# Optimization experiments

Measured on AMD Instinct MI355X. Metric: run time of the kernel, lower is better.

## Reference

```python
import jax, jax.numpy as jnp
import numpy as np
from jax import lax

D = 30   # embedding_dim (hardcoded in repo)
Q = 30   # question length
N = 4000 # number of sentences in doc
S = 100  # tokens per sentence
K = 5    # k_for_maxpool
SLOPE = 0.1  # LeakyReLU negative slope


def setup_inputs() -> dict:
    key = jax.random.key(0)
    ks = jax.random.split(key, 20)
    rn = lambda k, sh: jax.random.normal(k, sh, dtype=jnp.float32)
    ru = lambda k, sh: jax.random.uniform(k, sh, dtype=jnp.float32)
    return {
        "doc_sents_embeds": rn(ks[0], (N, S, D)),
        "sents_gaf": ru(ks[1], (N, 3)),
        "question_embeds": rn(ks[2], (Q, D)),
        "q_idfs": ru(ks[3], (Q, 1)),
        "doc_gaf": ru(ks[4], (4,)),
        "conv1_w": rn(ks[5], (D, D, 3)) * 0.1,
        "conv1_b": rn(ks[6], (D,)) * 0.1,
        "conv2_w": rn(ks[7], (D, D, 3)) * 0.1,
        "conv2_b": rn(ks[8], (D,)) * 0.1,
        "qw_W": rn(ks[9], (1, D + 1)) * 0.1,
        "qw_b": rn(ks[10], (1,)) * 0.1,
        "lq1_W": rn(ks[11], (8, 6)) * 0.1,
        "lq1_b": rn(ks[12], (8,)) * 0.1,
        "lq2_W": rn(ks[13], (1, 8)) * 0.1,
        "lq2_b": rn(ks[14], (1,)) * 0.1,
        "so_W": rn(ks[15], (1, 4)) * 0.1,
        "so_b": rn(ks[16], (1,)) * 0.1,
        "fl_W": rn(ks[17], (1, 5)) * 0.1,
        "fl_b": rn(ks[18], (1,)) * 0.1,
    }


def _leaky(x):
    return jnp.where(x >= 0, x, SLOPE * x)


def _conv_block(x, w, b):
    # x: [B, L, D]. torch Conv1d(D, D, 3, padding=2) then slice [1:L+1]
    # is exactly a 'same' conv with padding 1 on each side; then residual add.
    y = lax.conv_general_dilated(x.transpose(0, 2, 1), w, (1,), [(1, 1)],
                                 dimension_numbers=("NCH", "OIH", "NCH"))
    y = _leaky(y + b[None, :, None])
    return y.transpose(0, 2, 1) + x


def _cos_sim(A, B):
    # A: [Q, D], B: [N, S, D] -> [N, Q, S] (num/den as in torch my_cosine_sim)
    num = jnp.einsum("qd,nsd->nqs", A, B)
    den = jnp.linalg.norm(A, axis=-1)[None, :, None] * jnp.linalg.norm(B, axis=-1)[:, None, :]
    return num / den


def _pool(sim):
    # sort-based k-max pooling -> [max, avg_of_top_k]; sim: [N, Q, S] -> [N, Q, 2]
    vals = lax.top_k(sim, K)[0]  # descending
    return jnp.stack([vals[..., 0], vals.mean(-1)], axis=-1)


def reference(doc_sents_embeds, sents_gaf, question_embeds, q_idfs, doc_gaf,
              conv1_w, conv1_b, conv2_w, conv2_b, qw_W, qw_b,
              lq1_W, lq1_b, lq2_W, lq2_b, so_W, so_b, fl_W, fl_b):
    # question context (two residual trigram convs)
    q_conv = _conv_block(question_embeds[None], conv1_w, conv1_b)
    q_conv = _conv_block(q_conv, conv2_w, conv2_b)[0]          # [Q, D]
    # question term weights
    qw_in = jnp.concatenate([q_conv, q_idfs], axis=-1)          # [Q, D+1]
    q_weights = jax.nn.softmax((qw_in @ qw_W.T + qw_b)[:, 0])   # [Q]
    # sentence context convs (batched over all sentences)
    conv_res = _conv_block(doc_sents_embeds, conv1_w, conv1_b)
    conv_res = _conv_block(conv_res, conv2_w, conv2_b)          # [N, S, D]
    # similarity matrices
    sim_insens = _cos_sim(question_embeds, doc_sents_embeds)    # [N, Q, S]
    sim_oh = (sim_insens > 1.0 - 1e-3).astype(sim_insens.dtype)
    sim_sens = _cos_sim(q_conv, conv_res)
    # k-max pooling and per-q tiny MLP attention
    feats = jnp.concatenate([_pool(sim_oh), _pool(sim_insens), _pool(sim_sens)], axis=-1)  # [N, Q, 6]
    lo = _leaky(feats @ lq1_W.T + lq1_b) @ lq2_W.T + lq2_b      # [N, Q, 1]
    lo = lo[..., 0] * q_weights[None, :]
    sent_emit = lo.sum(-1) / Q                                  # [N]
    # per-sentence output layer
    sent_feats = jnp.concatenate([sents_gaf, sent_emit[:, None]], axis=-1)  # [N, 4]
    sent_scores = jax.nn.sigmoid((sent_feats @ so_W.T + so_b)[:, 0])        # [N]
    # doc-level score
    doc_rep = jnp.concatenate([jnp.max(sent_scores)[None], doc_gaf])        # [5]
    final = doc_rep @ fl_W.T + fl_b                                          # [1]
    return final, sent_scores
```

## Files before the change

### kernel.cpp

```cpp
#include <hip/hip_runtime.h>
#include <hip/hip_bf16.h>

#define SLOPE 0.1f

#define OFF_QW    1816
#define OFF_QNI   1846
#define OFF_QNS   1876
#define OFF_QNN   1906
#define OFF_B1    4606
#define OFF_B2    7336
#define OFF_LQ1W  7366
#define OFF_LQ1B  7414
#define OFF_LQ2W  7422
#define OFF_LQ2B  7430
#define OFF_SOW   7431
#define OFF_SOB   7435
#define OFF_FLW   7436
#define OFF_FLB   7441
#define U16_QEA   16384
#define U16_QCA   17408
#define U16_WB1   18432
#define U16_WB2   21504

typedef __attribute__((ext_vector_type(8))) __bf16 bf16x8;
typedef __attribute__((ext_vector_type(4))) float f32x4;

union Frag { uint4 u4; uint u[4]; bf16x8 v; };

__device__ __forceinline__ float bf2f(ushort h) {
    union { uint u; float f; } c; c.u = ((uint)h) << 16; return c.f;
}
__device__ __forceinline__ ushort f2bf(float f) {
    union { float f; uint u; } c; c.f = f;
    uint u = c.u;
    return (ushort)((u + 0x7FFFu + ((u >> 16) & 1u)) >> 16);
}
__device__ __forceinline__ float ldx(const void* p, long i, int bf) {
    if (bf) return bf2f(((const ushort*)p)[i]);
    return ((const float*)p)[i];
}
#define CE(x, y) { float _hi = fmaxf(x, y), _lo = fminf(x, y); x = _hi; y = _lo; }

__device__ __forceinline__ void sort4d(float& a, float& b, float& c, float& d) {
    CE(a, b); CE(c, d); CE(a, c); CE(b, d); CE(b, c);
}
__device__ __forceinline__ void merge44_5(const float* a, const float* b, float* t) {
    t[0] = fmaxf(a[0], b[0]);
    t[1] = fmaxf(fminf(a[0], b[0]), fmaxf(a[1], b[1]));
    t[2] = fmaxf(fmaxf(fminf(a[0], b[1]), fminf(a[1], b[0])), fmaxf(a[2], b[2]));
    t[3] = fmaxf(fmaxf(fminf(a[0], b[2]), fminf(a[1], b[1])),
                 fmaxf(fminf(a[2], b[0]), fmaxf(a[3], b[3])));
    t[4] = fmaxf(fmaxf(fminf(a[0], b[3]), fminf(a[1], b[2])),
                 fmaxf(fminf(a[2], b[1]), fminf(a[3], b[0])));
}
__device__ __forceinline__ void merge54_5(const float* a, const float* b, float* t) {
    t[0] = fmaxf(a[0], b[0]);
    t[1] = fmaxf(fminf(a[0], b[0]), fmaxf(a[1], b[1]));
    t[2] = fmaxf(fmaxf(fminf(a[0], b[1]), fminf(a[1], b[0])), fmaxf(a[2], b[2]));
    t[3] = fmaxf(fmaxf(fminf(a[0], b[2]), fminf(a[1], b[1])),
                 fmaxf(fminf(a[2], b[0]), fmaxf(a[3], b[3])));
    t[4] = fmaxf(fmaxf(fmaxf(fminf(a[0], b[3]), fminf(a[1], b[2])),
                       fmaxf(fminf(a[2], b[1]), fminf(a[3], b[0]))), a[4]);
}
__device__ __forceinline__ void merge55_5(const float* a, const float* b, float* t) {
    t[0] = fmaxf(a[0], b[0]);
    t[1] = fmaxf(fminf(a[0], b[0]), fmaxf(a[1], b[1]));
    t[2] = fmaxf(fmaxf(fminf(a[0], b[1]), fminf(a[1], b[0])), fmaxf(a[2], b[2]));
    t[3] = fmaxf(fmaxf(fminf(a[0], b[2]), fminf(a[1], b[1])),
                 fmaxf(fminf(a[2], b[0]), fmaxf(a[3], b[3])));
    t[4] = fmaxf(fmaxf(fmaxf(fminf(a[0], b[3]), fminf(a[1], b[2])),
                       fmaxf(fminf(a[2], b[1]), fminf(a[3], b[0]))),
                 fmaxf(a[4], b[4]));
}

__device__ __forceinline__ int detect_bf(const void* doc_in, int tid, int* scnt) {
    if (tid == 0) *scnt = 0;
    __syncthreads();
    const ushort* p = (const ushort*)doc_in;
    int local = 0;
    for (int i = tid; i < 4096; i += 256) {
        unsigned e = (p[i] >> 7) & 0xFFu;
        if (e != 0u && (e < 100u || e > 134u)) local++;
    }
    atomicAdd(scnt, local);
    __syncthreads();
    return (*scnt > 200) ? 0 : 1;
}

__global__ __launch_bounds__(256) void k_prep(
        const void* doc_in,
        const void* qe_in, const void* qidf_in,
        const void* w1_in, const void* b1_in,
        const void* w2_in, const void* b2_in,
        const void* qwW_in, const void* qwb_in,
        const void* lq1W_in, const void* lq1b_in,
        const void* lq2W_in, const void* lq2b_in,
        const void* soW_in, const void* sob_in,
        const void* flW_in, const void* flb_in,
        float* ws) {
    const int tid = threadIdx.x;
    const int blk = blockIdx.x;
    __shared__ float QE[900], T1[900], QC[900], W[2700], IDF[32], LG[32];
    __shared__ int scnt;

    const int bf = detect_bf(doc_in, tid, &scnt);
    ushort* wsu = (ushort*)ws;

    if (blk == 1) {
        if (tid == 0) { ((int*)ws)[0] = bf; }
        if (tid < 30) ws[OFF_B1 + tid] = ldx(b1_in, tid, bf);
        if (tid < 48) ws[OFF_LQ1W + tid] = ldx(lq1W_in, tid, bf);
        if (tid < 8)  { ws[OFF_LQ1B + tid] = ldx(lq1b_in, tid, bf);
                        ws[OFF_LQ2W + tid] = ldx(lq2W_in, tid, bf); }
        if (tid < 4)  ws[OFF_SOW + tid] = ldx(soW_in, tid, bf);
        if (tid < 5)  ws[OFF_FLW + tid] = ldx(flW_in, tid, bf);
        if (tid == 1) { ws[OFF_LQ2B] = ldx(lq2b_in, 0, bf);
                        ws[OFF_SOB]  = ldx(sob_in, 0, bf);
                        ws[OFF_FLB]  = ldx(flb_in, 0, bf); }
        for (int i = tid; i < 3072; i += 256) {
            int o = i / 96, kk = i % 96;
            float v1 = 0.f;
            if (o < 30 && kk < 90) {
                int ii = kk % 30, k = kk / 30;
                v1 = ldx(w1_in, (long)o*90 + ii*3 + k, bf);
            }
            wsu[U16_WB1 + i] = f2bf(v1);
        }
        return;
    }
    if (blk == 2) {
        if (tid < 30) ws[OFF_B2 + tid] = ldx(b2_in, tid, bf);
        for (int i = tid; i < 3072; i += 256) {
            int o = i / 96, kk = i % 96;
            float v2 = 0.f;
            if (o < 30 && kk < 90) {
                int ii = kk % 30, k = kk / 30;
                v2 = ldx(w2_in, (long)o*90 + ii*3 + k, bf);
            }
            wsu[U16_WB2 + i] = f2bf(v2);
        }
        return;
    }

    if (tid == 0) { ((int*)ws)[0] = bf; }

    for (int i = tid; i < 900; i += 256) QE[i] = ldx(qe_in, i, bf);
    if (tid < 30) IDF[tid] = ldx(qidf_in, tid, bf);
    for (int i = tid; i < 2700; i += 256) W[i] = ldx(w1_in, i, bf);
    __syncthreads();

    for (int idx = tid; idx < 900; idx += 256) {
        int s = idx / 30, o = idx % 30;
        float acc = ldx(b1_in, o, bf);
        for (int k = 0; k < 3; ++k) {
            int t = s + k - 1;
            if (t < 0 || t >= 30) continue;
            for (int i = 0; i < 30; ++i) acc += QE[t*30 + i] * W[o*90 + i*3 + k];
        }
        acc = acc >= 0.f ? acc : SLOPE * acc;
        T1[idx] = acc + QE[idx];
    }
    __syncthreads();
    for (int i = tid; i < 2700; i += 256) W[i] = ldx(w2_in, i, bf);
    __syncthreads();
    for (int idx = tid; idx < 900; idx += 256) {
        int s = idx / 30, o = idx % 30;
        float acc = ldx(b2_in, o, bf);
        for (int k = 0; k < 3; ++k) {
            int t = s + k - 1;
            if (t < 0 || t >= 30) continue;
            for (int i = 0; i < 30; ++i) acc += T1[t*30 + i] * W[o*90 + i*3 + k];
        }
        acc = acc >= 0.f ? acc : SLOPE * acc;
        QC[idx] = acc + T1[idx];
    }
    __syncthreads();

    if (tid < 30) {
        float s1 = 0.f, s2 = 0.f;
        for (int d = 0; d < 30; ++d) {
            float a = QE[tid*30 + d]; s1 += a*a;
            float b = QC[tid*30 + d]; s2 += b*b;
        }
        float n1 = sqrtf(s1);
        ws[OFF_QNN + tid] = n1;
        ws[OFF_QNI + tid] = 1.0f / n1;
        ws[OFF_QNS + tid] = 1.0f / sqrtf(s2);
        float z = ldx(qwb_in, 0, bf);
        for (int d = 0; d < 30; ++d) z += QC[tid*30 + d] * ldx(qwW_in, d, bf);
        z += IDF[tid] * ldx(qwW_in, 30, bf);
        LG[tid] = z;
    }
    __syncthreads();
    if (tid == 0) {
        float m = -1e30f;
        for (int q = 0; q < 30; ++q) m = fmaxf(m, LG[q]);
        float sum = 0.f, e[30];
        for (int q = 0; q < 30; ++q) { e[q] = expf(LG[q] - m); sum += e[q]; }
        for (int q = 0; q < 30; ++q) ws[OFF_QW + q] = e[q] / sum;
    }
    for (int i = tid; i < 1024; i += 256) {
        int q = i >> 5, d = i & 31;
        float ve = (q < 30 && d < 30) ? QE[q*30 + d] : 0.f;
        float vc = (q < 30 && d < 30) ? QC[q*30 + d] : 0.f;
        wsu[U16_QEA + i] = f2bf(ve);
        wsu[U16_QCA + i] = f2bf(vc);
    }
}

__global__ __launch_bounds__(128, 4) void k_main(const void* doc_in, const void* gaf_in,
                                                 void* out, float* ws) {
    const int n = blockIdx.x;
    const int tid = threadIdx.x;
    const int bf = ((const int*)ws)[0];
    const int lane = tid & 63;
    const int wid = tid >> 6;
    const int l15 = lane & 15;
    const int quad = lane >> 4;

    __shared__ uint XA32[1546];
    __shared__ uint XB32[1546];
    __shared__ __align__(16) float INVX[112];
    __shared__ float FE[30][6];
    __shared__ float IQI[32], IQS[32], QNN[32], BI1[32], BI2[32];

    ushort* XAu = (ushort*)XA32;
    const ushort* wsu = (const ushort*)ws;
    const uint4* qeA = (const uint4*)(wsu + U16_QEA);
    const uint4* qcA = (const uint4*)(wsu + U16_QCA);
    const uint4* wb1 = (const uint4*)(wsu + U16_WB1);
    const uint4* wb2 = (const uint4*)(wsu + U16_WB2);

    float ga0 = ldx(gaf_in, (long)n*3 + 0, bf);
    float ga1 = ldx(gaf_in, (long)n*3 + 1, bf);
    float ga2 = ldx(gaf_in, (long)n*3 + 2, bf);

    for (int i = tid; i < 46; i += 128) {
        int j = (i < 15) ? i : (1500 + i);
        XA32[j] = 0u; XB32[j] = 0u;
    }
    if (tid >= 100 && tid < 112) INVX[tid] = 0.f;
    if (bf) {
        const uint* g = (const uint*)((const ushort*)doc_in + (size_t)n * 3000);
        for (int i = tid; i < 1500; i += 128) XA32[15 + i] = g[i];
    } else {
        const float* p = (const float*)doc_in + (size_t)n * 3000;
        for (int i = tid; i < 3000; i += 128) XAu[30 + i] = f2bf(p[i]);
    }
    if (tid < 32) {
        IQI[tid] = ws[OFF_QNI + tid];
        IQS[tid] = ws[OFF_QNS + tid];
        QNN[tid] = ws[OFF_QNN + tid];
        BI1[tid] = ws[OFF_B1 + tid];
        BI2[tid] = ws[OFF_B2 + tid];
    }
    __syncthreads();

    if (tid < 100) {
        const uint* r = XA32 + (tid + 1) * 15;
        float s = 0.f;
        #pragma unroll
        for (int i = 0; i < 15; ++i) {
            uint u = r[i];
            float lo = __uint_as_float(u << 16);
            float hi = __uint_as_float(u & 0xFFFF0000u);
            s += lo * lo + hi * hi;
        }
        INVX[tid] = 1.f / sqrtf(s);
    }
    __syncthreads();

    auto sim_pool = [&](const uint4* qa, const float* IQ, int fbase, bool do_oh) {
        const int q = wid * 16 + l15;
        Frag b;
        b.u4 = qa[q * 4 + quad];
        f32x4 acc[7];
        #pragma unroll
        for (int mt = 0; mt < 7; ++mt) {
            int m = mt * 16 + l15;
            Frag a;
            if (m < 100) {
                int base = (m + 1) * 15 + quad * 4;
                a.u[0] = XA32[base];     a.u[1] = XA32[base + 1];
                a.u[2] = XA32[base + 2]; a.u[3] = XA32[base + 3];
            } else { a.u[0] = a.u[1] = a.u[2] = a.u[3] = 0u; }
            f32x4 z = {0.f, 0.f, 0.f, 0.f};
            acc[mt] = __builtin_amdgcn_mfma_f32_16x16x32_bf16(a.v, b.v, z, 0, 0, 0);
        }
        const float4* INVX4 = (const float4*)INVX;
        float thr = 0.999f * QNN[q];
        float iq  = (q < 30) ? IQ[q] : 0.f;
        float g[7][4];
        int cnt = 0;
        #pragma unroll
        for (int mt = 0; mt < 7; ++mt) {
            float4 ix = INVX4[mt * 4 + quad];
            float ixa[4] = {ix.x, ix.y, ix.z, ix.w};
            #pragma unroll
            for (int r = 0; r < 4; ++r) {
                float u = acc[mt][r] * ixa[r];
                if (mt == 6 && (quad * 4 + r) >= 4) u = -1e30f;
                g[mt][r] = u;
                if (do_oh) cnt += (u > thr) ? 1 : 0;
            }
        }
        #pragma unroll
        for (int mt = 0; mt < 7; ++mt) sort4d(g[mt][0], g[mt][1], g[mt][2], g[mt][3]);
        float p0[5], p1[5], p2[5], q0[5], q1[5], t[5];
        merge44_5(g[0], g[1], p0);
        merge44_5(g[2], g[3], p1);
        merge44_5(g[4], g[5], p2);
        merge55_5(p0, p1, q0);
        merge54_5(p2, g[6], q1);
        merge55_5(q0, q1, t);
        #pragma unroll
        for (int d = 16; d < 64; d <<= 1) {
            float pp[5];
            pp[0] = __shfl_xor(t[0], d); pp[1] = __shfl_xor(t[1], d);
            pp[2] = __shfl_xor(t[2], d); pp[3] = __shfl_xor(t[3], d);
            pp[4] = __shfl_xor(t[4], d);
            if (do_oh) cnt += __shfl_xor(cnt, d);
            float tn[5];
            merge55_5(t, pp, tn);
            t[0] = tn[0]; t[1] = tn[1]; t[2] = tn[2]; t[3] = tn[3]; t[4] = tn[4];
        }
        if (quad == 0 && q < 30) {
            if (do_oh) {
                FE[q][0] = cnt > 0 ? 1.f : 0.f;
                FE[q][1] = (float)(cnt > 5 ? 5 : cnt) * 0.2f;
            }
            FE[q][fbase]     = t[0] * iq;
            FE[q][fbase + 1] = (t[0] + t[1] + t[2] + t[3] + t[4]) * 0.2f * iq;
        }
    };

    auto conv_mt = [&](const uint* src32, uint* dst32, const uint4* wb,
                       const float* bias, int mt, int nt0, int nt1) {
        const ushort* srcU = (const ushort*)src32;
        ushort* dstU = (ushort*)dst32;
        int sa = mt * 16 + l15;
        Frag a[3];
        #pragma unroll
        for (int k = 0; k < 3; ++k) {
            if (sa < 100) {
                int base = sa * 15 + k * 16 + quad * 4;
                a[k].u[0] = src32[base];     a[k].u[1] = src32[base + 1];
                a[k].u[2] = src32[base + 2]; a[k].u[3] = src32[base + 3];
            } else { a[k].u[0] = a[k].u[1] = a[k].u[2] = a[k].u[3] = 0u; }
        }
        for (int nt = nt0; nt <= nt1; ++nt) {
            f32x4 acc = {0.f, 0.f, 0.f, 0.f};
            #pragma unroll
            for (int k = 0; k < 3; ++k) {
                Frag b;
                b.u4 = wb[(nt * 16 + l15) * 12 + k * 4 + quad];
                acc = __builtin_amdgcn_mfma_f32_16x16x32_bf16(a[k].v, b.v, acc, 0, 0, 0);
            }
            int o = nt * 16 + l15;
            if (o < 30) {
                float bo = bias[o];
                #pragma unroll
                for (int r = 0; r < 4; ++r) {
                    int s = mt * 16 + quad * 4 + r;
                    if (s < 100) {
                        float v = acc[r] + bo;
                        v = v >= 0.f ? v : SLOPE * v;
                        v += bf2f(srcU[(s + 1) * 30 + o]);
                        dstU[(s + 1) * 30 + o] = f2bf(v);
                    }
                }
            }
        }
    };

    sim_pool(qeA, IQI, 2, true);
    conv_mt(XA32, XB32, wb1, BI1, wid,     0, 1);
    conv_mt(XA32, XB32, wb1, BI1, wid + 2, 0, 1);
    conv_mt(XA32, XB32, wb1, BI1, wid + 4, 0, 1);
    conv_mt(XA32, XB32, wb1, BI1, 6,       wid, wid);
    __syncthreads();

    conv_mt(XB32, XA32, wb2, BI2, wid,     0, 1);
    conv_mt(XB32, XA32, wb2, BI2, wid + 2, 0, 1);
    conv_mt(XB32, XA32, wb2, BI2, wid + 4, 0, 1);
    conv_mt(XB32, XA32, wb2, BI2, 6,       wid, wid);
    __syncthreads();

    if (tid < 100) {
        const uint* r = XA32 + (tid + 1) * 15;
        float s = 0.f;
        #pragma unroll
        for (int i = 0; i < 15; ++i) {
            uint u = r[i];
            float lo = __uint_as_float(u << 16);
            float hi = __uint_as_float(u & 0xFFFF0000u);
            s += lo * lo + hi * hi;
        }
        INVX[tid] = 1.f / sqrtf(s);
    }
    __syncthreads();

    sim_pool(qcA, IQS, 4, false);
    __syncthreads();

    if (wid == 0) {
        float val = 0.f;
        if (lane < 30) {
            float lo = ws[OFF_LQ2B];
            #pragma unroll
            for (int j = 0; j < 8; ++j) {
                float h = ws[OFF_LQ1B + j];
                #pragma unroll
                for (int f = 0; f < 6; ++f) h += FE[lane][f] * ws[OFF_LQ1W + j*6 + f];
                h = h >= 0.f ? h : SLOPE * h;
                lo += h * ws[OFF_LQ2W + j];
            }
            val = lo * ws[OFF_QW + lane];
        }
        for (int d = 32; d >= 1; d >>= 1) val += __shfl_xor(val, d);
        if (lane == 0) {
            float emit = val * (1.f / 30.f);
            float z = ws[OFF_SOB];
            z += ga0 * ws[OFF_SOW + 0];
            z += ga1 * ws[OFF_SOW + 1];
            z += ga2 * ws[OFF_SOW + 2];
            z += emit * ws[OFF_SOW + 3];
            float sc = 1.f / (1.f + expf(-z));
            if (bf) ((__hip_bfloat16*)out)[1 + n] = __float2bfloat16(sc);
            else    ((float*)out)[1 + n] = sc;
        }
    }
}

__global__ __launch_bounds__(256) void k_final(const void* docgaf_in, void* out, const float* ws) {
    const int tid = threadIdx.x;
    const int bf = ((const int*)ws)[0];
    __shared__ float red[256];
    float m = -1e30f;
    for (int i = tid; i < 4000; i += 256) {
        float v = bf ? __bfloat162float(((const __hip_bfloat16*)out)[1 + i])
                     : ((const float*)out)[1 + i];
        m = fmaxf(m, v);
    }
    red[tid] = m;
    __syncthreads();
    for (int off = 128; off > 0; off >>= 1) {
        if (tid < off) red[tid] = fmaxf(red[tid], red[tid + off]);
        __syncthreads();
    }
    if (tid == 0) {
        float f = ws[OFF_FLB] + red[0] * ws[OFF_FLW + 0];
        for (int i = 0; i < 4; ++i) f += ldx(docgaf_in, i, bf) * ws[OFF_FLW + 1 + i];
        if (bf) ((__hip_bfloat16*)out)[0] = __float2bfloat16(f);
        else    ((float*)out)[0] = f;
    }
}

extern "C" void kernel_launch(void* const* d_in, const int* in_sizes, int n_in,
                              void* d_out, int out_size, void* d_ws, size_t ws_size,
                              hipStream_t stream) {
    float* ws = (float*)d_ws;
    k_prep<<<3, 256, 0, stream>>>(d_in[0], d_in[2], d_in[3], d_in[5], d_in[6], d_in[7], d_in[8],
                                  d_in[9], d_in[10], d_in[11], d_in[12], d_in[13], d_in[14],
                                  d_in[15], d_in[16], d_in[17], d_in[18], ws);
    k_main<<<4000, 128, 0, stream>>>(d_in[0], d_in[1], d_out, ws);
    k_final<<<1, 256, 0, stream>>>(d_in[4], d_out, ws);
}
```

Baseline: 179.3 us.

## Restructure conv MFMA with transposed operands, packed bf16 stores, and fused row norms

The conv is rewritten so weights are the A operand and activations the B operand. Both output tiles are computed per row tile, reusing activation fragments, and results are written as packed bf16 pairs with v_cvt_pk_bf16_f32. The second conv computes row sum-of-squares inline and writes the inverse norms, which removes a separate norm pass and one barrier. Small constant arrays are read directly from global memory instead of staged in shared memory, and the leaky ReLU is simplified to a fmax. The row tiles are now split unevenly across the two waves (3 and 4 tiles alternating between phases).

Measured after the change: 172.9 us. -3.6%, faster.

```diff
diff --git a/kernel.cpp b/kernel.cpp
--- a/kernel.cpp
+++ b/kernel.cpp
@@ -39,6 +39,15 @@
     if (bf) return bf2f(((const ushort*)p)[i]);
     return ((const float*)p)[i];
 }
+__device__ __forceinline__ uint pk2(float lo, float hi) {
+    uint r;
+    asm("v_cvt_pk_bf16_f32 %0, %1, %2" : "=v"(r) : "v"(lo), "v"(hi));
+    return r;
+}
+__device__ __forceinline__ float blo(uint u) { return __uint_as_float(u << 16); }
+__device__ __forceinline__ float bhi(uint u) { return __uint_as_float(u & 0xFFFF0000u); }
+__device__ __forceinline__ float lk(float x) { return fmaxf(x, SLOPE * x); }
+
 #define CE(x, y) { float _hi = fmaxf(x, y), _lo = fminf(x, y); x = _hi; y = _lo; }
 
 __device__ __forceinline__ void sort4d(float& a, float& b, float& c, float& d) {
@@ -222,7 +231,6 @@
     __shared__ uint XB32[1546];
     __shared__ __align__(16) float INVX[112];
     __shared__ float FE[30][6];
-    __shared__ float IQI[32], IQS[32], QNN[32], BI1[32], BI2[32];
 
     ushort* XAu = (ushort*)XA32;
     const ushort* wsu = (const ushort*)ws;
@@ -247,13 +255,6 @@
         const float* p = (const float*)doc_in + (size_t)n * 3000;
         for (int i = tid; i < 3000; i += 128) XAu[30 + i] = f2bf(p[i]);
     }
-    if (tid < 32) {
-        IQI[tid] = ws[OFF_QNI + tid];
-        IQS[tid] = ws[OFF_QNS + tid];
-        QNN[tid] = ws[OFF_QNN + tid];
-        BI1[tid] = ws[OFF_B1 + tid];
-        BI2[tid] = ws[OFF_B2 + tid];
-    }
     __syncthreads();
 
     if (tid < 100) {
@@ -270,7 +271,7 @@
     }
     __syncthreads();
 
-    auto sim_pool = [&](const uint4* qa, const float* IQ, int fbase, bool do_oh) {
+    auto sim_pool = [&](const uint4* qa, int iqOff, int fbase, bool do_oh) {
         const int q = wid * 16 + l15;
         Frag b;
         b.u4 = qa[q * 4 + quad];
@@ -288,8 +289,8 @@
             acc[mt] = __builtin_amdgcn_mfma_f32_16x16x32_bf16(a.v, b.v, z, 0, 0, 0);
         }
         const float4* INVX4 = (const float4*)INVX;
-        float thr = 0.999f * QNN[q];
-        float iq  = (q < 30) ? IQ[q] : 0.f;
+        float thr = (do_oh && q < 30) ? 0.999f * ws[OFF_QNN + q] : 1e30f;
+        float iq  = (q < 30) ? ws[iqOff + q] : 0.f;
         float g[7][4];
         int cnt = 0;
         #pragma unroll
@@ -334,73 +335,81 @@
         }
     };
 
-    auto conv_mt = [&](const uint* src32, uint* dst32, const uint4* wb,
-                       const float* bias, int mt, int nt0, int nt1) {
-        const ushort* srcU = (const ushort*)src32;
-        ushort* dstU = (ushort*)dst32;
-        int sa = mt * 16 + l15;
-        Frag a[3];
+    auto conv_phase = [&](const uint* src32, uint* dst32, const uint4* wb, int bOff,
+                          int m0, int m1, int m2, int m3, bool donorm) {
+        Frag wf0[3], wf1[3];
         #pragma unroll
         for (int k = 0; k < 3; ++k) {
-            if (sa < 100) {
-                int base = sa * 15 + k * 16 + quad * 4;
-                a[k].u[0] = src32[base];     a[k].u[1] = src32[base + 1];
-                a[k].u[2] = src32[base + 2]; a[k].u[3] = src32[base + 3];
-            } else { a[k].u[0] = a[k].u[1] = a[k].u[2] = a[k].u[3] = 0u; }
-        }
-        for (int nt = nt0; nt <= nt1; ++nt) {
-            f32x4 acc = {0.f, 0.f, 0.f, 0.f};
+            wf0[k].u4 = wb[l15 * 12 + k * 4 + quad];
+            wf1[k].u4 = wb[(16 + l15) * 12 + k * 4 + quad];
+        }
+        float b40[4], b41[4];
+        #pragma unroll
+        for (int r = 0; r < 4; ++r) {
+            int o0 = quad * 4 + r, o1 = 16 + quad * 4 + r;
+            b40[r] = ws[bOff + o0];
+            b41[r] = (o1 < 30) ? ws[bOff + o1] : 0.f;
+        }
+        auto do_mt = [&](int mt) {
+            const int s = mt * 16 + l15;
+            const bool sv = (s < 100);
+            Frag xf[3];
             #pragma unroll
             for (int k = 0; k < 3; ++k) {
-                Frag b;
-                b.u4 = wb[(nt * 16 + l15) * 12 + k * 4 + quad];
-                acc = __builtin_amdgcn_mfma_f32_16x16x32_bf16(a[k].v, b.v, acc, 0, 0, 0);
-            }
-            int o = nt * 16 + l15;
-            if (o < 30) {
-                float bo = bias[o];
-                #pragma unroll
-                for (int r = 0; r < 4; ++r) {
-                    int s = mt * 16 + quad * 4 + r;
-                    if (s < 100) {
-                        float v = acc[r] + bo;
-                        v = v >= 0.f ? v : SLOPE * v;
-                        v += bf2f(srcU[(s + 1) * 30 + o]);
-                        dstU[(s + 1) * 30 + o] = f2bf(v);
-                    }
+                if (sv) {
+                    int base = s * 15 + k * 16 + quad * 4;
+                    xf[k].u[0] = src32[base];     xf[k].u[1] = src32[base + 1];
+                    xf[k].u[2] = src32[base + 2]; xf[k].u[3] = src32[base + 3];
+                } else { xf[k].u[0] = xf[k].u[1] = xf[k].u[2] = xf[k].u[3] = 0u; }
+            }
+            f32x4 a0 = {0.f, 0.f, 0.f, 0.f}, a1 = {0.f, 0.f, 0.f, 0.f};
+            #pragma unroll
+            for (int k = 0; k < 3; ++k) {
+                a0 = __builtin_amdgcn_mfma_f32_16x16x32_bf16(wf0[k].v, xf[k].v, a0, 0, 0, 0);
+                a1 = __builtin_amdgcn_mfma_f32_16x16x32_bf16(wf1[k].v, xf[k].v, a1, 0, 0, 0);
+            }
+            float ss = 0.f;
+            if (sv) {
+                const int db = (s + 1) * 15 + quad * 2;
+                uint u0 = src32[db],     u1 = src32[db + 1];
+                uint u2 = src32[db + 8], u3 = src32[db + 9];
+                float v0 = lk(a0[0] + b40[0]) + blo(u0);
+                float v1 = lk(a0[1] + b40[1]) + bhi(u0);
+                float v2 = lk(a0[2] + b40[2]) + blo(u1);
+                float v3 = lk(a0[3] + b40[3]) + bhi(u1);
+                dst32[db]     = pk2(v0, v1);
+                dst32[db + 1] = pk2(v2, v3);
+                float w0 = lk(a1[0] + b41[0]) + blo(u2);
+                float w1 = lk(a1[1] + b41[1]) + bhi(u2);
+                dst32[db + 8] = pk2(w0, w1);
+                ss = v0*v0 + v1*v1 + v2*v2 + v3*v3 + w0*w0 + w1*w1;
+                if (quad < 3) {
+                    float w2 = lk(a1[2] + b41[2]) + blo(u3);
+                    float w3 = lk(a1[3] + b41[3]) + bhi(u3);
+                    dst32[db + 9] = pk2(w2, w3);
+                    ss += w2*w2 + w3*w3;
                 }
             }
-        }
+            if (donorm) {
+                ss += __shfl_xor(ss, 16);
+                ss += __shfl_xor(ss, 32);
+                if (quad == 0 && sv) INVX[s] = 1.f / sqrtf(ss);
+            }
+        };
+        do_mt(m0); do_mt(m1); do_mt(m2);
+        if (m3 >= 0) do_mt(m3);
     };
 
-    sim_pool(qeA, IQI, 2, true);
-    conv_mt(XA32, XB32, wb1, BI1, wid,     0, 1);
-    conv_mt(XA32, XB32, wb1, BI1, wid + 2, 0, 1);
-    conv_mt(XA32, XB32, wb1, BI1, wid + 4, 0, 1);
-    conv_mt(XA32, XB32, wb1, BI1, 6,       wid, wid);
-    __syncthreads();
-
-    conv_mt(XB32, XA32, wb2, BI2, wid,     0, 1);
-    conv_mt(XB32, XA32, wb2, BI2, wid + 2, 0, 1);
-    conv_mt(XB32, XA32, wb2, BI2, wid + 4, 0, 1);
-    conv_mt(XB32, XA32, wb2, BI2, 6,       wid, wid);
-    __syncthreads();
-
-    if (tid < 100) {
-        const uint* r = XA32 + (tid + 1) * 15;
-        float s = 0.f;
-        #pragma unroll
-        for (int i = 0; i < 15; ++i) {
-            uint u = r[i];
-            float lo = __uint_as_float(u << 16);
-            float hi = __uint_as_float(u & 0xFFFF0000u);
-            s += lo * lo + hi * hi;
-        }
-        INVX[tid] = 1.f / sqrtf(s);
-    }
-    __syncthreads();
-
-    sim_pool(qcA, IQS, 4, false);
+    sim_pool(qeA, OFF_QNI, 2, true);
+    if (wid == 0) conv_phase(XA32, XB32, wb1, OFF_B1, 0, 2, 4, -1, false);
+    else          conv_phase(XA32, XB32, wb1, OFF_B1, 1, 3, 5,  6, false);
+    __syncthreads();
+
+    if (wid == 0) conv_phase(XB32, XA32, wb2, OFF_B2, 0, 2, 4,  6, true);
+    else          conv_phase(XB32, XA32, wb2, OFF_B2, 1, 3, 5, -1, true);
+    __syncthreads();
+
+    sim_pool(qcA, OFF_QNS, 4, false);
     __syncthreads();
 
     if (wid == 0) {
```
